# Optimization experiments

Measured on AMD Instinct MI355X. Metric: run time of the kernel, lower is better.

The kernel has to match this reference:

```python
import jax, jax.numpy as jnp
import numpy as np

E = 64          # num_routed_experts
K = 6           # num_experts_per_token
NS = 2          # num_shared_experts
D = 512         # hidden_size
F = 512         # expert_intermediate_size = intermediate_size // 4


def setup_inputs() -> dict:
    key = jax.random.key(0)
    ks = jax.random.split(key, 8)
    s = 0.02
    return {
        "hidden_states": jax.random.normal(ks[0], (2, 1024, D), dtype=jnp.float32),
        "Wr": jax.random.normal(ks[1], (D, E), dtype=jnp.float32) * s,      # router
        "sWg": jax.random.normal(ks[2], (NS, D, F), dtype=jnp.float32) * s,  # shared gate_proj
        "sWu": jax.random.normal(ks[3], (NS, D, F), dtype=jnp.float32) * s,  # shared up_proj
        "sWd": jax.random.normal(ks[4], (NS, F, D), dtype=jnp.float32) * s,  # shared down_proj
        "Wg": jax.random.normal(ks[5], (E, D, F), dtype=jnp.float32) * s,    # routed gate_proj
        "Wu": jax.random.normal(ks[6], (E, D, F), dtype=jnp.float32) * s,    # routed up_proj
        "Wd": jax.random.normal(ks[7], (E, F, D), dtype=jnp.float32) * s,    # routed down_proj
    }


def _swiglu_ffn(x, wg, wu, wd):
    # x: (N, D); wg/wu: (D, F); wd: (F, D)
    return (jax.nn.silu(x @ wg) * (x @ wu)) @ wd


def reference(hidden_states, Wr, sWg, sWu, sWd, Wg, Wu, Wd):
    B, S, d = hidden_states.shape
    x = hidden_states.reshape(-1, d)  # (N, D)
    N = x.shape[0]

    # ---- shared experts (always on) ----
    shared = jnp.zeros_like(x)
    for e in range(NS):
        shared = shared + _swiglu_ffn(x, sWg[e], sWu[e], sWd[e])

    # ---- top-k router ----
    logits = x @ Wr                                   # (N, E)
    probs = jax.nn.softmax(logits, axis=-1)
    top_w, top_i = jax.lax.top_k(probs, K)            # (N, K)
    top_w = top_w / jnp.sum(top_w, axis=-1, keepdims=True)  # renormalize
    gate = jnp.zeros((N, E), dtype=x.dtype).at[jnp.arange(N)[:, None], top_i].set(top_w)

    # ---- routed experts: per-expert FFN, combined with sparse gate ----
    routed = jnp.zeros_like(x)
    for e in range(E):
        routed = routed + _swiglu_ffn(x, Wg[e], Wu[e], Wd[e]) * gate[:, e:e + 1]

    out = (shared + routed + x).reshape(B, S, d)
    return out
```

## Files before the change

### kernel.cpp

```cpp
#include <hip/hip_runtime.h>

#define N_TOK 2048
#define DD 512
#define FF 512
#define EE 64
#define TK 6
#define NG 66
#define RSLOT 12288
#define NSLOT 16384
#define BM 64
#define BN 64

typedef float f32x4 __attribute__((ext_vector_type(4)));
typedef __bf16 bf16x8 __attribute__((ext_vector_type(8)));
typedef short s16x8 __attribute__((ext_vector_type(8)));

__device__ __forceinline__ short f2bf(float f) {
  unsigned u = __builtin_bit_cast(unsigned, f);
  u = (u + 0x7fffu + ((u >> 16) & 1u)) >> 16;
  return (short)u;
}

__global__ void router_k(const float* __restrict__ x, const float* __restrict__ Wr,
                         int* __restrict__ top_i, float* __restrict__ top_w,
                         int* __restrict__ cnt) {
  int wave = threadIdx.x >> 6, lane = threadIdx.x & 63;
  int t0 = (blockIdx.x * 4 + wave) * 4;
  const float* x0 = x + (size_t)t0 * DD;
  float a0 = 0.f, a1 = 0.f, a2 = 0.f, a3 = 0.f;
  for (int k = 0; k < DD; ++k) {
    float wv = Wr[k * EE + lane];
    a0 = fmaf(x0[k], wv, a0);
    a1 = fmaf(x0[DD + k], wv, a1);
    a2 = fmaf(x0[2 * DD + k], wv, a2);
    a3 = fmaf(x0[3 * DD + k], wv, a3);
  }
  float accs[4] = {a0, a1, a2, a3};
#pragma unroll
  for (int tt = 0; tt < 4; ++tt) {
    int t = t0 + tt;
    float acc = accs[tt];
    float m = acc;
#pragma unroll
    for (int s = 32; s; s >>= 1) m = fmaxf(m, __shfl_xor(m, s));
    float p = __expf(acc - m);
    int wi[TK]; float wv[TK];
#pragma unroll
    for (int it = 0; it < TK; ++it) {
      float v = p;
#pragma unroll
      for (int s = 32; s; s >>= 1) v = fmaxf(v, __shfl_xor(v, s));
      unsigned long long b = __ballot(p == v);
      int idx = __ffsll((unsigned long long)b) - 1;
      wi[it] = idx; wv[it] = v;
      if (lane == idx) p = -1.f;
    }
    float wsum = 0.f;
#pragma unroll
    for (int it = 0; it < TK; ++it) wsum += wv[it];
    if (lane < TK) {
      int si = 0; float sv = 0.f;
#pragma unroll
      for (int it = 0; it < TK; ++it) if (lane == it) { si = wi[it]; sv = wv[it]; }
      top_i[t * TK + lane] = si;
      top_w[t * TK + lane] = sv / wsum;
      atomicAdd(&cnt[si], 1);
    }
  }
}

__global__ void offsets_k(const int* __restrict__ cnt, int* __restrict__ goff,
                          int* __restrict__ fill) {
  int i = threadIdx.x;
  if (i < EE) fill[i] = 0;
  if (i == 0) {
    int s = 0;
    for (int e = 0; e < EE; ++e) { goff[e] = s; s += cnt[e]; }
    goff[EE] = RSLOT;
    goff[EE + 1] = RSLOT + N_TOK;
    goff[EE + 2] = RSLOT + 2 * N_TOK;
  }
}

__global__ void scatter_k(const int* __restrict__ top_i, const float* __restrict__ top_w,
                          const int* __restrict__ goff, int* __restrict__ fill,
                          int* __restrict__ btok, float* __restrict__ bw) {
  int idx = blockIdx.x * blockDim.x + threadIdx.x;
  if (idx < RSLOT) {
    int e = top_i[idx];
    int pos = goff[e] + atomicAdd(&fill[e], 1);
    btok[pos] = idx / TK;
    bw[pos] = top_w[idx];
  } else if (idx < NSLOT) {
    int j = idx - RSLOT;
    btok[idx] = j & (N_TOK - 1);
    bw[idx] = 1.0f;
  }
}

__global__ void initout_k(const float* __restrict__ x, float* __restrict__ out, int n4) {
  int i = blockIdx.x * blockDim.x + threadIdx.x;
  if (i < n4) reinterpret_cast<f32x4*>(out)[i] = reinterpret_cast<const f32x4*>(x)[i];
}

__global__ __launch_bounds__(256) void gemm1_k(
    const float* __restrict__ x, const float* __restrict__ Wg, const float* __restrict__ Wu,
    const float* __restrict__ sWg, const float* __restrict__ sWu,
    const int* __restrict__ goff, const int* __restrict__ btok,
    short* __restrict__ H) {
  int g = blockIdx.z;
  int s0g = goff[g], cnt = goff[g + 1] - s0g;
  int mt = blockIdx.y;
  if (mt * BM >= cnt) return;
  int n0 = blockIdx.x * BN;
  const float* wgp = (g < EE) ? Wg + (size_t)g * DD * FF : sWg + (size_t)(g - EE) * DD * FF;
  const float* wup = (g < EE) ? Wu + (size_t)g * DD * FF : sWu + (size_t)(g - EE) * DD * FF;

  __shared__ short laA[4][BM][8];
  __shared__ short lbG[4][BN][8];
  __shared__ short lbU[4][BN][8];

  int tid = threadIdx.x;
  int lane = tid & 63;
  int w = tid >> 6;
  int wr = w >> 1, wc = w & 1;
  int lr = lane & 15, lgq = lane >> 4;

  int sm = tid >> 2, skb = tid & 3;
  int sn = tid & 63, skb2 = tid >> 6;

  int s0 = s0g + mt * BM;
  int tok = btok[((mt * BM + sm) < cnt) ? (s0 + sm) : s0];
  const float* xrow = x + (size_t)tok * DD;

  f32x4 accg[2][2], accu[2][2];
#pragma unroll
  for (int i = 0; i < 2; ++i)
#pragma unroll
    for (int j = 0; j < 2; ++j) {
      accg[i][j] = f32x4{0.f, 0.f, 0.f, 0.f};
      accu[i][j] = f32x4{0.f, 0.f, 0.f, 0.f};
    }

  for (int kt = 0; kt < DD / 32; ++kt) {
    int k0 = kt * 32;
    __syncthreads();
    {
      const float* p = xrow + k0 + skb * 8;
      f32x4 v0 = *reinterpret_cast<const f32x4*>(p);
      f32x4 v1 = *reinterpret_cast<const f32x4*>(p + 4);
      s16x8 o;
      o[0] = f2bf(v0[0]); o[1] = f2bf(v0[1]); o[2] = f2bf(v0[2]); o[3] = f2bf(v0[3]);
      o[4] = f2bf(v1[0]); o[5] = f2bf(v1[1]); o[6] = f2bf(v1[2]); o[7] = f2bf(v1[3]);
      *reinterpret_cast<s16x8*>(&laA[skb][sm][0]) = o;
    }
    {
      const float* bgp = wgp + (size_t)(k0 + skb2 * 8) * FF + n0 + sn;
      const float* bup = wup + (size_t)(k0 + skb2 * 8) * FF + n0 + sn;
      s16x8 og, ou;
#pragma unroll
      for (int i = 0; i < 8; ++i) {
        og[i] = f2bf(bgp[(size_t)i * FF]);
        ou[i] = f2bf(bup[(size_t)i * FF]);
      }
      *reinterpret_cast<s16x8*>(&lbG[skb2][sn][0]) = og;
      *reinterpret_cast<s16x8*>(&lbU[skb2][sn][0]) = ou;
    }
    __syncthreads();
    bf16x8 af[2], bgf[2], buf[2];
#pragma unroll
    for (int i = 0; i < 2; ++i)
      af[i] = *reinterpret_cast<const bf16x8*>(&laA[lgq][wr * 32 + i * 16 + lr][0]);
#pragma unroll
    for (int j = 0; j < 2; ++j) {
      bgf[j] = *reinterpret_cast<const bf16x8*>(&lbG[lgq][wc * 32 + j * 16 + lr][0]);
      buf[j] = *reinterpret_cast<const bf16x8*>(&lbU[lgq][wc * 32 + j * 16 + lr][0]);
    }
#pragma unroll
    for (int i = 0; i < 2; ++i)
#pragma unroll
      for (int j = 0; j < 2; ++j) {
        accg[i][j] = __builtin_amdgcn_mfma_f32_16x16x32_bf16(af[i], bgf[j], accg[i][j], 0, 0, 0);
        accu[i][j] = __builtin_amdgcn_mfma_f32_16x16x32_bf16(af[i], buf[j], accu[i][j], 0, 0, 0);
      }
  }
#pragma unroll
  for (int i = 0; i < 2; ++i)
#pragma unroll
    for (int j = 0; j < 2; ++j)
#pragma unroll
      for (int r = 0; r < 4; ++r) {
        int mrow = wr * 32 + i * 16 + lgq * 4 + r;
        if (mt * BM + mrow < cnt) {
          float gg = accg[i][j][r];
          float uu = accu[i][j][r];
          float hv = (gg / (1.f + __expf(-gg))) * uu;
          int col = n0 + wc * 32 + j * 16 + lr;
          H[(size_t)(s0 + mrow) * FF + col] = f2bf(hv);
        }
      }
}

__global__ __launch_bounds__(256) void gemm2_k(
    const short* __restrict__ H, const float* __restrict__ Wd, const float* __restrict__ sWd,
    const int* __restrict__ goff, const int* __restrict__ btok, const float* __restrict__ bw,
    float* __restrict__ out) {
  int g = blockIdx.z;
  int s0g = goff[g], cnt = goff[g + 1] - s0g;
  int mt = blockIdx.y;
  if (mt * BM >= cnt) return;
  int n0 = blockIdx.x * BN;
  const float* wdp = (g < EE) ? Wd + (size_t)g * FF * DD : sWd + (size_t)(g - EE) * FF * DD;

  __shared__ short laA[4][BM][8];
  __shared__ short lbB[4][BN][8];

  int tid = threadIdx.x;
  int lane = tid & 63;
  int w = tid >> 6;
  int wr = w >> 1, wc = w & 1;
  int lr = lane & 15, lgq = lane >> 4;

  int sm = tid >> 2, skb = tid & 3;
  int sn = tid & 63, skb2 = tid >> 6;

  int s0 = s0g + mt * BM;
  int srow = s0 + sm;
  if (srow > NSLOT - 1) srow = NSLOT - 1;
  const short* hrow = H + (size_t)srow * FF;

  f32x4 acc[2][2];
#pragma unroll
  for (int i = 0; i < 2; ++i)
#pragma unroll
    for (int j = 0; j < 2; ++j) acc[i][j] = f32x4{0.f, 0.f, 0.f, 0.f};

  for (int kt = 0; kt < FF / 32; ++kt) {
    int k0 = kt * 32;
    __syncthreads();
    {
      s16x8 v = *reinterpret_cast<const s16x8*>(hrow + k0 + skb * 8);
      *reinterpret_cast<s16x8*>(&laA[skb][sm][0]) = v;
    }
    {
      const float* bp = wdp + (size_t)(k0 + skb2 * 8) * DD + n0 + sn;
      s16x8 ob;
#pragma unroll
      for (int i = 0; i < 8; ++i) ob[i] = f2bf(bp[(size_t)i * DD]);
      *reinterpret_cast<s16x8*>(&lbB[skb2][sn][0]) = ob;
    }
    __syncthreads();
    bf16x8 af[2], bf[2];
#pragma unroll
    for (int i = 0; i < 2; ++i)
      af[i] = *reinterpret_cast<const bf16x8*>(&laA[lgq][wr * 32 + i * 16 + lr][0]);
#pragma unroll
    for (int j = 0; j < 2; ++j)
      bf[j] = *reinterpret_cast<const bf16x8*>(&lbB[lgq][wc * 32 + j * 16 + lr][0]);
#pragma unroll
    for (int i = 0; i < 2; ++i)
#pragma unroll
      for (int j = 0; j < 2; ++j)
        acc[i][j] = __builtin_amdgcn_mfma_f32_16x16x32_bf16(af[i], bf[j], acc[i][j], 0, 0, 0);
  }
#pragma unroll
  for (int i = 0; i < 2; ++i)
#pragma unroll
    for (int j = 0; j < 2; ++j)
#pragma unroll
      for (int r = 0; r < 4; ++r) {
        int mrow = wr * 32 + i * 16 + lgq * 4 + r;
        if (mt * BM + mrow < cnt) {
          int slot = s0 + mrow;
          int tok = btok[slot];
          float wv = bw[slot];
          int col = n0 + wc * 32 + j * 16 + lr;
          atomicAdd(&out[(size_t)tok * DD + col], acc[i][j][r] * wv);
        }
      }
}

extern "C" void kernel_launch(void* const* d_in, const int* in_sizes, int n_in,
                              void* d_out, int out_size, void* d_ws, size_t ws_size,
                              hipStream_t stream) {
  const float* x   = (const float*)d_in[0];
  const float* Wr  = (const float*)d_in[1];
  const float* sWg = (const float*)d_in[2];
  const float* sWu = (const float*)d_in[3];
  const float* sWd = (const float*)d_in[4];
  const float* Wg  = (const float*)d_in[5];
  const float* Wu  = (const float*)d_in[6];
  const float* Wd  = (const float*)d_in[7];
  float* out = (float*)d_out;

  char* wsb = (char*)d_ws;
  size_t off = 0;
  short* H = (short*)(wsb + off);    off += (size_t)NSLOT * FF * 2;
  int*   top_i = (int*)(wsb + off);  off += (size_t)RSLOT * 4;
  float* top_w = (float*)(wsb + off); off += (size_t)RSLOT * 4;
  int*   btok = (int*)(wsb + off);   off += (size_t)NSLOT * 4;
  float* bwt  = (float*)(wsb + off); off += (size_t)NSLOT * 4;
  int*   cnt  = (int*)(wsb + off);   off += 256;
  int*   fill = (int*)(wsb + off);   off += 256;
  int*   goff = (int*)(wsb + off);   off += 256;

  hipMemsetAsync(cnt, 0, 256, stream);
  router_k<<<N_TOK / 16, 256, 0, stream>>>(x, Wr, top_i, top_w, cnt);
  offsets_k<<<1, 64, 0, stream>>>(cnt, goff, fill);
  scatter_k<<<NSLOT / 256, 256, 0, stream>>>(top_i, top_w, goff, fill, btok, bwt);
  int n4 = out_size / 4;
  initout_k<<<(n4 + 255) / 256, 256, 0, stream>>>(x, out, n4);
  dim3 grid1(FF / BN, N_TOK / BM, NG);
  gemm1_k<<<grid1, 256, 0, stream>>>(x, Wg, Wu, sWg, sWu, goff, btok, H);
  dim3 grid2(DD / BN, N_TOK / BM, NG);
  gemm2_k<<<grid2, 256, 0, stream>>>(H, Wd, sWd, goff, btok, bwt, out);
}
```

Before: 211.3 us.

## Double-buffer LDS and enlarge M tile to 128 in both expert GEMMs

```diff
diff --git a/kernel.cpp b/kernel.cpp
--- a/kernel.cpp
+++ b/kernel.cpp
@@ -8,8 +8,8 @@
 #define NG 66
 #define RSLOT 12288
 #define NSLOT 16384
-#define BM 64
-#define BN 64
+#define BM1 128
+#define BN1 64
 
 typedef float f32x4 __attribute__((ext_vector_type(4)));
 typedef __bf16 bf16x8 __attribute__((ext_vector_type(8)));
@@ -111,91 +111,113 @@
   int g = blockIdx.z;
   int s0g = goff[g], cnt = goff[g + 1] - s0g;
   int mt = blockIdx.y;
-  if (mt * BM >= cnt) return;
-  int n0 = blockIdx.x * BN;
+  if (mt * BM1 >= cnt) return;
+  int n0 = blockIdx.x * BN1;
   const float* wgp = (g < EE) ? Wg + (size_t)g * DD * FF : sWg + (size_t)(g - EE) * DD * FF;
   const float* wup = (g < EE) ? Wu + (size_t)g * DD * FF : sWu + (size_t)(g - EE) * DD * FF;
 
-  __shared__ short laA[4][BM][8];
-  __shared__ short lbG[4][BN][8];
-  __shared__ short lbU[4][BN][8];
+  __shared__ short laA[2][4][BM1][8];
+  __shared__ short lbG[2][4][BN1][8];
+  __shared__ short lbU[2][4][BN1][8];
 
   int tid = threadIdx.x;
   int lane = tid & 63;
   int w = tid >> 6;
-  int wr = w >> 1, wc = w & 1;
   int lr = lane & 15, lgq = lane >> 4;
 
-  int sm = tid >> 2, skb = tid & 3;
-  int sn = tid & 63, skb2 = tid >> 6;
-
-  int s0 = s0g + mt * BM;
-  int tok = btok[((mt * BM + sm) < cnt) ? (s0 + sm) : s0];
-  const float* xrow = x + (size_t)tok * DD;
-
-  f32x4 accg[2][2], accu[2][2];
+  int arow = tid >> 1, ahalf = tid & 1;
+  int bcol = tid & 63, bkp = tid >> 6;
+
+  int s0 = s0g + mt * BM1;
+  int aslot = (mt * BM1 + arow < cnt) ? s0 + arow : s0;
+  const float* xrow = x + (size_t)btok[aslot] * DD + ahalf * 16;
+  const float* gbase = wgp + n0 + bcol;
+  const float* ubase = wup + n0 + bcol;
+
+  f32x4 accg[2][4], accu[2][4];
 #pragma unroll
   for (int i = 0; i < 2; ++i)
 #pragma unroll
-    for (int j = 0; j < 2; ++j) {
+    for (int j = 0; j < 4; ++j) {
       accg[i][j] = f32x4{0.f, 0.f, 0.f, 0.f};
       accu[i][j] = f32x4{0.f, 0.f, 0.f, 0.f};
     }
 
+  f32x4 ar0, ar1, ar2, ar3;
+  float og[8], ou[8];
+
+  auto LOAD = [&](int kt) {
+    const float* p = xrow + kt * 32;
+    ar0 = *reinterpret_cast<const f32x4*>(p);
+    ar1 = *reinterpret_cast<const f32x4*>(p + 4);
+    ar2 = *reinterpret_cast<const f32x4*>(p + 8);
+    ar3 = *reinterpret_cast<const f32x4*>(p + 12);
+    int kb = kt * 32 + bkp * 8;
+#pragma unroll
+    for (int i = 0; i < 8; ++i) {
+      og[i] = gbase[(size_t)(kb + i) * FF];
+      ou[i] = ubase[(size_t)(kb + i) * FF];
+    }
+  };
+  auto STORE = [&](int b) {
+    s16x8 o0, o1;
+    o0[0] = f2bf(ar0[0]); o0[1] = f2bf(ar0[1]); o0[2] = f2bf(ar0[2]); o0[3] = f2bf(ar0[3]);
+    o0[4] = f2bf(ar1[0]); o0[5] = f2bf(ar1[1]); o0[6] = f2bf(ar1[2]); o0[7] = f2bf(ar1[3]);
+    o1[0] = f2bf(ar2[0]); o1[1] = f2bf(ar2[1]); o1[2] = f2bf(ar2[2]); o1[3] = f2bf(ar2[3]);
+    o1[4] = f2bf(ar3[0]); o1[5] = f2bf(ar3[1]); o1[6] = f2bf(ar3[2]); o1[7] = f2bf(ar3[3]);
+    *reinterpret_cast<s16x8*>(&laA[b][2 * ahalf][arow][0]) = o0;
+    *reinterpret_cast<s16x8*>(&laA[b][2 * ahalf + 1][arow][0]) = o1;
+    s16x8 cg, cu;
+#pragma unroll
+    for (int i = 0; i < 8; ++i) { cg[i] = f2bf(og[i]); cu[i] = f2bf(ou[i]); }
+    *reinterpret_cast<s16x8*>(&lbG[b][bkp][bcol][0]) = cg;
+    *reinterpret_cast<s16x8*>(&lbU[b][bkp][bcol][0]) = cu;
+  };
+  auto COMPUTE = [&](int b) {
+    bf16x8 af[2], bg[4], bu[4];
+#pragma unroll
+    for (int i = 0; i < 2; ++i)
+      af[i] = *reinterpret_cast<const bf16x8*>(&laA[b][lgq][w * 32 + i * 16 + lr][0]);
+#pragma unroll
+    for (int j = 0; j < 4; ++j) {
+      bg[j] = *reinterpret_cast<const bf16x8*>(&lbG[b][lgq][j * 16 + lr][0]);
+      bu[j] = *reinterpret_cast<const bf16x8*>(&lbU[b][lgq][j * 16 + lr][0]);
+    }
+#pragma unroll
+    for (int i = 0; i < 2; ++i)
+#pragma unroll
+      for (int j = 0; j < 4; ++j) {
+        accg[i][j] = __builtin_amdgcn_mfma_f32_16x16x32_bf16(af[i], bg[j], accg[i][j], 0, 0, 0);
+        accu[i][j] = __builtin_amdgcn_mfma_f32_16x16x32_bf16(af[i], bu[j], accu[i][j], 0, 0, 0);
+      }
+  };
+
+  LOAD(0);
+  STORE(0);
+  __syncthreads();
+#pragma unroll 1
   for (int kt = 0; kt < DD / 32; ++kt) {
-    int k0 = kt * 32;
-    __syncthreads();
-    {
-      const float* p = xrow + k0 + skb * 8;
-      f32x4 v0 = *reinterpret_cast<const f32x4*>(p);
-      f32x4 v1 = *reinterpret_cast<const f32x4*>(p + 4);
-      s16x8 o;
-      o[0] = f2bf(v0[0]); o[1] = f2bf(v0[1]); o[2] = f2bf(v0[2]); o[3] = f2bf(v0[3]);
-      o[4] = f2bf(v1[0]); o[5] = f2bf(v1[1]); o[6] = f2bf(v1[2]); o[7] = f2bf(v1[3]);
-      *reinterpret_cast<s16x8*>(&laA[skb][sm][0]) = o;
-    }
-    {
-      const float* bgp = wgp + (size_t)(k0 + skb2 * 8) * FF + n0 + sn;
-      const float* bup = wup + (size_t)(k0 + skb2 * 8) * FF + n0 + sn;
-      s16x8 og, ou;
-#pragma unroll
-      for (int i = 0; i < 8; ++i) {
-        og[i] = f2bf(bgp[(size_t)i * FF]);
-        ou[i] = f2bf(bup[(size_t)i * FF]);
-      }
-      *reinterpret_cast<s16x8*>(&lbG[skb2][sn][0]) = og;
-      *reinterpret_cast<s16x8*>(&lbU[skb2][sn][0]) = ou;
-    }
-    __syncthreads();
-    bf16x8 af[2], bgf[2], buf[2];
-#pragma unroll
-    for (int i = 0; i < 2; ++i)
-      af[i] = *reinterpret_cast<const bf16x8*>(&laA[lgq][wr * 32 + i * 16 + lr][0]);
-#pragma unroll
-    for (int j = 0; j < 2; ++j) {
-      bgf[j] = *reinterpret_cast<const bf16x8*>(&lbG[lgq][wc * 32 + j * 16 + lr][0]);
-      buf[j] = *reinterpret_cast<const bf16x8*>(&lbU[lgq][wc * 32 + j * 16 + lr][0]);
-    }
-#pragma unroll
-    for (int i = 0; i < 2; ++i)
-#pragma unroll
-      for (int j = 0; j < 2; ++j) {
-        accg[i][j] = __builtin_amdgcn_mfma_f32_16x16x32_bf16(af[i], bgf[j], accg[i][j], 0, 0, 0);
-        accu[i][j] = __builtin_amdgcn_mfma_f32_16x16x32_bf16(af[i], buf[j], accu[i][j], 0, 0, 0);
-      }
-  }
+    int cur = kt & 1;
+    if (kt < DD / 32 - 1) LOAD(kt + 1);
+    COMPUTE(cur);
+    if (kt < DD / 32 - 1) {
+      STORE(cur ^ 1);
+      __syncthreads();
+    }
+  }
+
 #pragma unroll
   for (int i = 0; i < 2; ++i)
 #pragma unroll
-    for (int j = 0; j < 2; ++j)
+    for (int j = 0; j < 4; ++j)
 #pragma unroll
       for (int r = 0; r < 4; ++r) {
-        int mrow = wr * 32 + i * 16 + lgq * 4 + r;
-        if (mt * BM + mrow < cnt) {
+        int mrow = w * 32 + i * 16 + lgq * 4 + r;
+        if (mt * BM1 + mrow < cnt) {
           float gg = accg[i][j][r];
           float uu = accu[i][j][r];
           float hv = (gg / (1.f + __expf(-gg))) * uu;
-          int col = n0 + wc * 32 + j * 16 + lr;
+          int col = n0 + j * 16 + lr;
           H[(size_t)(s0 + mrow) * FF + col] = f2bf(hv);
         }
       }
@@ -208,76 +230,96 @@
   int g = blockIdx.z;
   int s0g = goff[g], cnt = goff[g + 1] - s0g;
   int mt = blockIdx.y;
-  if (mt * BM >= cnt) return;
-  int n0 = blockIdx.x * BN;
+  if (mt * BM1 >= cnt) return;
+  int n0 = blockIdx.x * BN1;
   const float* wdp = (g < EE) ? Wd + (size_t)g * FF * DD : sWd + (size_t)(g - EE) * FF * DD;
 
-  __shared__ short laA[4][BM][8];
-  __shared__ short lbB[4][BN][8];
+  __shared__ short laA[2][4][BM1][8];
+  __shared__ short lbB[2][4][BN1][8];
 
   int tid = threadIdx.x;
   int lane = tid & 63;
   int w = tid >> 6;
-  int wr = w >> 1, wc = w & 1;
   int lr = lane & 15, lgq = lane >> 4;
 
-  int sm = tid >> 2, skb = tid & 3;
-  int sn = tid & 63, skb2 = tid >> 6;
-
-  int s0 = s0g + mt * BM;
-  int srow = s0 + sm;
-  if (srow > NSLOT - 1) srow = NSLOT - 1;
-  const short* hrow = H + (size_t)srow * FF;
-
-  f32x4 acc[2][2];
+  int arow = tid >> 1, ahalf = tid & 1;
+  int bcol = tid & 63, bkp = tid >> 6;
+
+  int s0 = s0g + mt * BM1;
+  int aslot = (mt * BM1 + arow < cnt) ? s0 + arow : s0;
+  const short* hrow = H + (size_t)aslot * FF + ahalf * 16;
+  const float* dbase = wdp + n0 + bcol;
+
+  f32x4 acc[2][4];
 #pragma unroll
   for (int i = 0; i < 2; ++i)
 #pragma unroll
-    for (int j = 0; j < 2; ++j) acc[i][j] = f32x4{0.f, 0.f, 0.f, 0.f};
-
+    for (int j = 0; j < 4; ++j) acc[i][j] = f32x4{0.f, 0.f, 0.f, 0.f};
+
+  s16x8 h0, h1;
+  float od[8];
+
+  auto LOAD = [&](int kt) {
+    const short* p = hrow + kt * 32;
+    h0 = *reinterpret_cast<const s16x8*>(p);
+    h1 = *reinterpret_cast<const s16x8*>(p + 8);
+    int kb = kt * 32 + bkp * 8;
+#pragma unroll
+    for (int i = 0; i < 8; ++i) od[i] = dbase[(size_t)(kb + i) * DD];
+  };
+  auto STORE = [&](int b) {
+    *reinterpret_cast<s16x8*>(&laA[b][2 * ahalf][arow][0]) = h0;
+    *reinterpret_cast<s16x8*>(&laA[b][2 * ahalf + 1][arow][0]) = h1;
+    s16x8 cd;
+#pragma unroll
+    for (int i = 0; i < 8; ++i) cd[i] = f2bf(od[i]);
+    *reinterpret_cast<s16x8*>(&lbB[b][bkp][bcol][0]) = cd;
+  };
+  auto COMPUTE = [&](int b) {
+    bf16x8 af[2], bd[4];
+#pragma unroll
+    for (int i = 0; i < 2; ++i)
+      af[i] = *reinterpret_cast<const bf16x8*>(&laA[b][lgq][w * 32 + i * 16 + lr][0]);
+#pragma unroll
+    for (int j = 0; j < 4; ++j)
+      bd[j] = *reinterpret_cast<const bf16x8*>(&lbB[b][lgq][j * 16 + lr][0]);
+#pragma unroll
+    for (int i = 0; i < 2; ++i)
+#pragma unroll
+      for (int j = 0; j < 4; ++j)
+        acc[i][j] = __builtin_amdgcn_mfma_f32_16x16x32_bf16(af[i], bd[j], acc[i][j], 0, 0, 0);
+  };
+
+  LOAD(0);
+  STORE(0);
+  __syncthreads();
+#pragma unroll 1
   for (int kt = 0; kt < FF / 32; ++kt) {
-    int k0 = kt * 32;
-    __syncthreads();
-    {
-      s16x8 v = *reinterpret_cast<const s16x8*>(hrow + k0 + skb * 8);
-      *reinterpret_cast<s16x8*>(&laA[skb][sm][0]) = v;
-    }
-    {
-      const float* bp = wdp + (size_t)(k0 + skb2 * 8) * DD + n0 + sn;
-      s16x8 ob;
-#pragma unroll
-      for (int i = 0; i < 8; ++i) ob[i] = f2bf(bp[(size_t)i * DD]);
-      *reinterpret_cast<s16x8*>(&lbB[skb2][sn][0]) = ob;
-    }
-    __syncthreads();
-    bf16x8 af[2], bf[2];
-#pragma unroll
-    for (int i = 0; i < 2; ++i)
-      af[i] = *reinterpret_cast<const bf16x8*>(&laA[lgq][wr * 32 + i * 16 + lr][0]);
-#pragma unroll
-    for (int j = 0; j < 2; ++j)
-      bf[j] = *reinterpret_cast<const bf16x8*>(&lbB[lgq][wc * 32 + j * 16 + lr][0]);
-#pragma unroll
-    for (int i = 0; i < 2; ++i)
-#pragma unroll
-      for (int j = 0; j < 2; ++j)
-        acc[i][j] = __builtin_amdgcn_mfma_f32_16x16x32_bf16(af[i], bf[j], acc[i][j], 0, 0, 0);
-  }
+    int cur = kt & 1;
+    if (kt < FF / 32 - 1) LOAD(kt + 1);
+    COMPUTE(cur);
+    if (kt < FF / 32 - 1) {
+      STORE(cur ^ 1);
+      __syncthreads();
+    }
+  }
+
 #pragma unroll
   for (int i = 0; i < 2; ++i)
 #pragma unroll
-    for (int j = 0; j < 2; ++j)
-#pragma unroll
-      for (int r = 0; r < 4; ++r) {
-        int mrow = wr * 32 + i * 16 + lgq * 4 + r;
-        if (mt * BM + mrow < cnt) {
-          int slot = s0 + mrow;
-          int tok = btok[slot];
-          float wv = bw[slot];
-          int col = n0 + wc * 32 + j * 16 + lr;
+    for (int r = 0; r < 4; ++r) {
+      int mrow = w * 32 + i * 16 + lgq * 4 + r;
+      if (mt * BM1 + mrow < cnt) {
+        int slot = s0 + mrow;
+        int tok = btok[slot];
+        float wv = bw[slot];
+#pragma unroll
+        for (int j = 0; j < 4; ++j) {
+          int col = n0 + j * 16 + lr;
           atomicAdd(&out[(size_t)tok * DD + col], acc[i][j][r] * wv);
         }
       }
+    }
 }
 
 extern "C" void kernel_launch(void* const* d_in, const int* in_sizes, int n_in,
@@ -310,8 +352,8 @@
   scatter_k<<<NSLOT / 256, 256, 0, stream>>>(top_i, top_w, goff, fill, btok, bwt);
   int n4 = out_size / 4;
   initout_k<<<(n4 + 255) / 256, 256, 0, stream>>>(x, out, n4);
-  dim3 grid1(FF / BN, N_TOK / BM, NG);
+  dim3 grid1(FF / BN1, (N_TOK + BM1 - 1) / BM1, NG);
   gemm1_k<<<grid1, 256, 0, stream>>>(x, Wg, Wu, sWg, sWu, goff, btok, H);
-  dim3 grid2(DD / BN, N_TOK / BM, NG);
+  dim3 grid2(DD / BN1, (N_TOK + BM1 - 1) / BM1, NG);
   gemm2_k<<<grid2, 256, 0, stream>>>(H, Wd, sWd, goff, btok, bwt, out);
 }
```

Measured after the change: 245.5 us. 16.2% more time.

## Double-buffer LDS tiles with register prefetch and use packed bf16 conversion

Applied to the files above, without the earlier changes.

```diff
diff --git a/kernel.cpp b/kernel.cpp
--- a/kernel.cpp
+++ b/kernel.cpp
@@ -10,15 +10,17 @@
 #define NSLOT 16384
 #define BM 64
 #define BN 64
+#define NT1 (DD / 32)
+#define NT2 (FF / 32)
 
 typedef float f32x4 __attribute__((ext_vector_type(4)));
 typedef __bf16 bf16x8 __attribute__((ext_vector_type(8)));
 typedef short s16x8 __attribute__((ext_vector_type(8)));
 
-__device__ __forceinline__ short f2bf(float f) {
-  unsigned u = __builtin_bit_cast(unsigned, f);
-  u = (u + 0x7fffu + ((u >> 16) & 1u)) >> 16;
-  return (short)u;
+__device__ __forceinline__ unsigned cvtpk(float lo, float hi) {
+  unsigned r;
+  asm("v_cvt_pk_bf16_f32 %0, %1, %2" : "=v"(r) : "v"(lo), "v"(hi));
+  return r;
 }
 
 __global__ void router_k(const float* __restrict__ x, const float* __restrict__ Wr,
@@ -116,9 +118,9 @@
   const float* wgp = (g < EE) ? Wg + (size_t)g * DD * FF : sWg + (size_t)(g - EE) * DD * FF;
   const float* wup = (g < EE) ? Wu + (size_t)g * DD * FF : sWu + (size_t)(g - EE) * DD * FF;
 
-  __shared__ short laA[4][BM][8];
-  __shared__ short lbG[4][BN][8];
-  __shared__ short lbU[4][BN][8];
+  __shared__ short laA[2][4][BM][8];
+  __shared__ short lbG[2][4][BN][8];
+  __shared__ short lbU[2][4][BN][8];
 
   int tid = threadIdx.x;
   int lane = tid & 63;
@@ -126,12 +128,14 @@
   int wr = w >> 1, wc = w & 1;
   int lr = lane & 15, lgq = lane >> 4;
 
-  int sm = tid >> 2, skb = tid & 3;
-  int sn = tid & 63, skb2 = tid >> 6;
+  int arow = tid >> 2, aseg = tid & 3;
+  int bcol = tid & 63, bkp = tid >> 6;
 
   int s0 = s0g + mt * BM;
-  int tok = btok[((mt * BM + sm) < cnt) ? (s0 + sm) : s0];
-  const float* xrow = x + (size_t)tok * DD;
+  int aslot = (mt * BM + arow < cnt) ? s0 + arow : s0;
+  const float* xrow = x + (size_t)btok[aslot] * DD + aseg * 8;
+  const float* gb = wgp + n0 + bcol;
+  const float* ub = wup + n0 + bcol;
 
   f32x4 accg[2][2], accu[2][2];
 #pragma unroll
@@ -142,48 +146,72 @@
       accu[i][j] = f32x4{0.f, 0.f, 0.f, 0.f};
     }
 
-  for (int kt = 0; kt < DD / 32; ++kt) {
-    int k0 = kt * 32;
+  f32x4 a0_0, a0_1, a1_0, a1_1;
+  float g0[8], u0[8], g1[8], u1[8];
+
+#define LOAD1(S, kt) do { \
+    const float* _p = xrow + (kt) * 32; \
+    a##S##_0 = *reinterpret_cast<const f32x4*>(_p); \
+    a##S##_1 = *reinterpret_cast<const f32x4*>(_p + 4); \
+    int _kb = (kt) * 32 + bkp * 8; \
+    _Pragma("unroll") \
+    for (int _i = 0; _i < 8; ++_i) { \
+      g##S[_i] = gb[(size_t)((_kb + _i) * FF)]; \
+      u##S[_i] = ub[(size_t)((_kb + _i) * FF)]; \
+    } \
+  } while (0)
+
+#define STORE1(S, b) do { \
+    uint4 _va; \
+    _va.x = cvtpk(a##S##_0[0], a##S##_0[1]); _va.y = cvtpk(a##S##_0[2], a##S##_0[3]); \
+    _va.z = cvtpk(a##S##_1[0], a##S##_1[1]); _va.w = cvtpk(a##S##_1[2], a##S##_1[3]); \
+    *reinterpret_cast<uint4*>(&laA[b][aseg][arow][0]) = _va; \
+    uint4 _vg, _vu; \
+    _vg.x = cvtpk(g##S[0], g##S[1]); _vg.y = cvtpk(g##S[2], g##S[3]); \
+    _vg.z = cvtpk(g##S[4], g##S[5]); _vg.w = cvtpk(g##S[6], g##S[7]); \
+    _vu.x = cvtpk(u##S[0], u##S[1]); _vu.y = cvtpk(u##S[2], u##S[3]); \
+    _vu.z = cvtpk(u##S[4], u##S[5]); _vu.w = cvtpk(u##S[6], u##S[7]); \
+    *reinterpret_cast<uint4*>(&lbG[b][bkp][bcol][0]) = _vg; \
+    *reinterpret_cast<uint4*>(&lbU[b][bkp][bcol][0]) = _vu; \
+  } while (0)
+
+#define COMPUTE1(b) do { \
+    bf16x8 _af[2], _bg[2], _bu[2]; \
+    _Pragma("unroll") \
+    for (int _i = 0; _i < 2; ++_i) \
+      _af[_i] = *reinterpret_cast<const bf16x8*>(&laA[b][lgq][wr * 32 + _i * 16 + lr][0]); \
+    _Pragma("unroll") \
+    for (int _j = 0; _j < 2; ++_j) { \
+      _bg[_j] = *reinterpret_cast<const bf16x8*>(&lbG[b][lgq][wc * 32 + _j * 16 + lr][0]); \
+      _bu[_j] = *reinterpret_cast<const bf16x8*>(&lbU[b][lgq][wc * 32 + _j * 16 + lr][0]); \
+    } \
+    _Pragma("unroll") \
+    for (int _i = 0; _i < 2; ++_i) \
+      _Pragma("unroll") \
+      for (int _j = 0; _j < 2; ++_j) { \
+        accg[_i][_j] = __builtin_amdgcn_mfma_f32_16x16x32_bf16(_af[_i], _bg[_j], accg[_i][_j], 0, 0, 0); \
+        accu[_i][_j] = __builtin_amdgcn_mfma_f32_16x16x32_bf16(_af[_i], _bu[_j], accu[_i][_j], 0, 0, 0); \
+      } \
+  } while (0)
+
+  LOAD1(0, 0);
+  LOAD1(1, 1);
+  STORE1(0, 0);
+  __syncthreads();
+#pragma unroll 1
+  for (int kt = 0; kt < NT1; kt += 2) {
+    if (kt + 2 < NT1) LOAD1(0, kt + 2);
+    COMPUTE1(0);
+    STORE1(1, 1);
     __syncthreads();
-    {
-      const float* p = xrow + k0 + skb * 8;
-      f32x4 v0 = *reinterpret_cast<const f32x4*>(p);
-      f32x4 v1 = *reinterpret_cast<const f32x4*>(p + 4);
-      s16x8 o;
-      o[0] = f2bf(v0[0]); o[1] = f2bf(v0[1]); o[2] = f2bf(v0[2]); o[3] = f2bf(v0[3]);
-      o[4] = f2bf(v1[0]); o[5] = f2bf(v1[1]); o[6] = f2bf(v1[2]); o[7] = f2bf(v1[3]);
-      *reinterpret_cast<s16x8*>(&laA[skb][sm][0]) = o;
-    }
-    {
-      const float* bgp = wgp + (size_t)(k0 + skb2 * 8) * FF + n0 + sn;
-      const float* bup = wup + (size_t)(k0 + skb2 * 8) * FF + n0 + sn;
-      s16x8 og, ou;
-#pragma unroll
-      for (int i = 0; i < 8; ++i) {
-        og[i] = f2bf(bgp[(size_t)i * FF]);
-        ou[i] = f2bf(bup[(size_t)i * FF]);
-      }
-      *reinterpret_cast<s16x8*>(&lbG[skb2][sn][0]) = og;
-      *reinterpret_cast<s16x8*>(&lbU[skb2][sn][0]) = ou;
+    if (kt + 3 < NT1) LOAD1(1, kt + 3);
+    COMPUTE1(1);
+    if (kt + 2 < NT1) {
+      STORE1(0, 0);
     }
     __syncthreads();
-    bf16x8 af[2], bgf[2], buf[2];
-#pragma unroll
-    for (int i = 0; i < 2; ++i)
-      af[i] = *reinterpret_cast<const bf16x8*>(&laA[lgq][wr * 32 + i * 16 + lr][0]);
-#pragma unroll
-    for (int j = 0; j < 2; ++j) {
-      bgf[j] = *reinterpret_cast<const bf16x8*>(&lbG[lgq][wc * 32 + j * 16 + lr][0]);
-      buf[j] = *reinterpret_cast<const bf16x8*>(&lbU[lgq][wc * 32 + j * 16 + lr][0]);
-    }
-#pragma unroll
-    for (int i = 0; i < 2; ++i)
-#pragma unroll
-      for (int j = 0; j < 2; ++j) {
-        accg[i][j] = __builtin_amdgcn_mfma_f32_16x16x32_bf16(af[i], bgf[j], accg[i][j], 0, 0, 0);
-        accu[i][j] = __builtin_amdgcn_mfma_f32_16x16x32_bf16(af[i], buf[j], accu[i][j], 0, 0, 0);
-      }
-  }
+  }
+
 #pragma unroll
   for (int i = 0; i < 2; ++i)
 #pragma unroll
@@ -196,9 +224,12 @@
           float uu = accu[i][j][r];
           float hv = (gg / (1.f + __expf(-gg))) * uu;
           int col = n0 + wc * 32 + j * 16 + lr;
-          H[(size_t)(s0 + mrow) * FF + col] = f2bf(hv);
+          H[(size_t)(s0 + mrow) * FF + col] = (short)(cvtpk(hv, hv) & 0xffffu);
         }
       }
+#undef LOAD1
+#undef STORE1
+#undef COMPUTE1
 }
 
 __global__ __launch_bounds__(256) void gemm2_k(
@@ -212,8 +243,8 @@
   int n0 = blockIdx.x * BN;
   const float* wdp = (g < EE) ? Wd + (size_t)g * FF * DD : sWd + (size_t)(g - EE) * FF * DD;
 
-  __shared__ short laA[4][BM][8];
-  __shared__ short lbB[4][BN][8];
+  __shared__ short laA[2][4][BM][8];
+  __shared__ short lbB[2][4][BN][8];
 
   int tid = threadIdx.x;
   int lane = tid & 63;
@@ -221,13 +252,13 @@
   int wr = w >> 1, wc = w & 1;
   int lr = lane & 15, lgq = lane >> 4;
 
-  int sm = tid >> 2, skb = tid & 3;
-  int sn = tid & 63, skb2 = tid >> 6;
+  int arow = tid >> 2, aseg = tid & 3;
+  int bcol = tid & 63, bkp = tid >> 6;
 
   int s0 = s0g + mt * BM;
-  int srow = s0 + sm;
-  if (srow > NSLOT - 1) srow = NSLOT - 1;
-  const short* hrow = H + (size_t)srow * FF;
+  int aslot = (mt * BM + arow < cnt) ? s0 + arow : s0;
+  const short* hrow = H + (size_t)aslot * FF + aseg * 8;
+  const float* db = wdp + n0 + bcol;
 
   f32x4 acc[2][2];
 #pragma unroll
@@ -235,49 +266,76 @@
 #pragma unroll
     for (int j = 0; j < 2; ++j) acc[i][j] = f32x4{0.f, 0.f, 0.f, 0.f};
 
-  for (int kt = 0; kt < FF / 32; ++kt) {
-    int k0 = kt * 32;
+  uint4 h0, h1;
+  float d0[8], d1[8];
+
+#define LOAD2(S, kt) do { \
+    h##S = *reinterpret_cast<const uint4*>(hrow + (kt) * 32); \
+    int _kb = (kt) * 32 + bkp * 8; \
+    _Pragma("unroll") \
+    for (int _i = 0; _i < 8; ++_i) d##S[_i] = db[(size_t)((_kb + _i) * DD)]; \
+  } while (0)
+
+#define STORE2(S, b) do { \
+    *reinterpret_cast<uint4*>(&laA[b][aseg][arow][0]) = h##S; \
+    uint4 _vd; \
+    _vd.x = cvtpk(d##S[0], d##S[1]); _vd.y = cvtpk(d##S[2], d##S[3]); \
+    _vd.z = cvtpk(d##S[4], d##S[5]); _vd.w = cvtpk(d##S[6], d##S[7]); \
+    *reinterpret_cast<uint4*>(&lbB[b][bkp][bcol][0]) = _vd; \
+  } while (0)
+
+#define COMPUTE2(b) do { \
+    bf16x8 _af[2], _bd[2]; \
+    _Pragma("unroll") \
+    for (int _i = 0; _i < 2; ++_i) \
+      _af[_i] = *reinterpret_cast<const bf16x8*>(&laA[b][lgq][wr * 32 + _i * 16 + lr][0]); \
+    _Pragma("unroll") \
+    for (int _j = 0; _j < 2; ++_j) \
+      _bd[_j] = *reinterpret_cast<const bf16x8*>(&lbB[b][lgq][wc * 32 + _j * 16 + lr][0]); \
+    _Pragma("unroll") \
+    for (int _i = 0; _i < 2; ++_i) \
+      _Pragma("unroll") \
+      for (int _j = 0; _j < 2; ++_j) \
+        acc[_i][_j] = __builtin_amdgcn_mfma_f32_16x16x32_bf16(_af[_i], _bd[_j], acc[_i][_j], 0, 0, 0); \
+  } while (0)
+
+  LOAD2(0, 0);
+  LOAD2(1, 1);
+  STORE2(0, 0);
+  __syncthreads();
+#pragma unroll 1
+  for (int kt = 0; kt < NT2; kt += 2) {
+    if (kt + 2 < NT2) LOAD2(0, kt + 2);
+    COMPUTE2(0);
+    STORE2(1, 1);
     __syncthreads();
-    {
-      s16x8 v = *reinterpret_cast<const s16x8*>(hrow + k0 + skb * 8);
-      *reinterpret_cast<s16x8*>(&laA[skb][sm][0]) = v;
-    }
-    {
-      const float* bp = wdp + (size_t)(k0 + skb2 * 8) * DD + n0 + sn;
-      s16x8 ob;
-#pragma unroll
-      for (int i = 0; i < 8; ++i) ob[i] = f2bf(bp[(size_t)i * DD]);
-      *reinterpret_cast<s16x8*>(&lbB[skb2][sn][0]) = ob;
+    if (kt + 3 < NT2) LOAD2(1, kt + 3);
+    COMPUTE2(1);
+    if (kt + 2 < NT2) {
+      STORE2(0, 0);
     }
     __syncthreads();
-    bf16x8 af[2], bf[2];
-#pragma unroll
-    for (int i = 0; i < 2; ++i)
-      af[i] = *reinterpret_cast<const bf16x8*>(&laA[lgq][wr * 32 + i * 16 + lr][0]);
-#pragma unroll
-    for (int j = 0; j < 2; ++j)
-      bf[j] = *reinterpret_cast<const bf16x8*>(&lbB[lgq][wc * 32 + j * 16 + lr][0]);
-#pragma unroll
-    for (int i = 0; i < 2; ++i)
-#pragma unroll
-      for (int j = 0; j < 2; ++j)
-        acc[i][j] = __builtin_amdgcn_mfma_f32_16x16x32_bf16(af[i], bf[j], acc[i][j], 0, 0, 0);
-  }
+  }
+
 #pragma unroll
   for (int i = 0; i < 2; ++i)
 #pragma unroll
-    for (int j = 0; j < 2; ++j)
-#pragma unroll
-      for (int r = 0; r < 4; ++r) {
-        int mrow = wr * 32 + i * 16 + lgq * 4 + r;
-        if (mt * BM + mrow < cnt) {
-          int slot = s0 + mrow;
-          int tok = btok[slot];
-          float wv = bw[slot];
+    for (int r = 0; r < 4; ++r) {
+      int mrow = wr * 32 + i * 16 + lgq * 4 + r;
+      if (mt * BM + mrow < cnt) {
+        int slot = s0 + mrow;
+        int tok = btok[slot];
+        float wv = bw[slot];
+#pragma unroll
+        for (int j = 0; j < 2; ++j) {
           int col = n0 + wc * 32 + j * 16 + lr;
           atomicAdd(&out[(size_t)tok * DD + col], acc[i][j][r] * wv);
         }
       }
+    }
+#undef LOAD2
+#undef STORE2
+#undef COMPUTE2
 }
 
 extern "C" void kernel_launch(void* const* d_in, const int* in_sizes, int n_in,
```

Measured after the change: 199.7 us. 5.5% less time.
